# Performance work log

Hardware: AMD Instinct MI355X
Metric: run time of the kernel (lower is better)

Reference implementation:

```python
import jax, jax.numpy as jnp
import numpy as np


def setup_inputs() -> dict:
    key = jax.random.key(0)
    ks = jax.random.split(key, 7)
    B, T, IN_F = 16384, 64, 48
    F = 32          # feature_size = len(INTERACTIVE_LIST)
    H = 128         # embedding_hidden_size
    TF, TH = T * F, T * H
    scale1 = 1.0 / np.sqrt(TF)
    scale2 = 1.0 / np.sqrt(TH)
    return {
        "x": jax.random.normal(ks[0], (B, T, IN_F), dtype=jnp.float32),
        "W1": jax.random.normal(ks[1], (TF, TH), dtype=jnp.float32) * scale1,
        "b1": jax.random.normal(ks[2], (TH,), dtype=jnp.float32) * scale1,
        "W2": jax.random.normal(ks[3], (TH, TF), dtype=jnp.float32) * scale2,
        "b2": jax.random.normal(ks[4], (TF,), dtype=jnp.float32) * scale2,
        "weight": jax.random.normal(ks[5], (T, F), dtype=jnp.float32),
        "bias": jax.random.normal(ks[6], (F,), dtype=jnp.float32) * (1.0 / np.sqrt(T)),
        "sample_index": jnp.arange(F, dtype=jnp.int32),
    }


def reference(x, W1, b1, W2, b2, weight, bias, sample_index):
    # x: [B, T, IN_F]; gather interactive feature columns -> [B, T, F]
    B = x.shape[0]
    T, F = weight.shape
    xs = jnp.take(x, sample_index, axis=2)            # [B, T, F]
    # pass_linear=True path: MLP on flattened time*feature vector
    h = jax.nn.relu(xs.reshape(B, T * F) @ W1 + b1)   # [B, T*H]; dropout = identity (eval)
    out = (h @ W2 + b2).reshape(B, T, F)              # [B, T, F]
    # vectorized form of the per-sample loop: sum over time of elementwise mul
    emb = jnp.einsum("btf,tf->bf", out, weight) + bias  # [B, F]
    return emb
```

## Files before the change

kernel.cpp:

```cpp
#include <hip/hip_runtime.h>
#include <hip/hip_bf16.h>

#define BATCH 16384
#define TT    64
#define INF   48
#define FF    32
#define TFD   2048
#define THD   8192

typedef __attribute__((ext_vector_type(8))) short bf16x8;
typedef __attribute__((ext_vector_type(4))) short bf16x4;
typedef __attribute__((ext_vector_type(4))) short short4v;
typedef __attribute__((ext_vector_type(4))) float f32x4;

#define SCHED __builtin_amdgcn_sched_barrier(0)
#define VMW(n) asm volatile("s_waitcnt vmcnt(" #n ")" ::: "memory")
#define LGKM0  asm volatile("s_waitcnt lgkmcnt(0)" ::: "memory")

__device__ inline void gload_lds16(const void* g, void* l) {
  __builtin_amdgcn_global_load_lds((const __attribute__((address_space(1))) void*)g,
                                   (__attribute__((address_space(3))) void*)l, 16, 0, 0);
}

__device__ inline f32x4 mfma16x16x16_bf16(bf16x4 a, bf16x4 b, f32x4 c) {
#if __has_builtin(__builtin_amdgcn_mfma_f32_16x16x16bf16_1k)
  return __builtin_amdgcn_mfma_f32_16x16x16bf16_1k(a, b, c, 0, 0, 0);
#else
  asm("v_mfma_f32_16x16x16_bf16 %0, %1, %2, %0" : "+v"(c) : "v"(a), "v"(b));
  return c;
#endif
}

__device__ inline short f32_to_bf16_bits(float x) {
  __hip_bfloat16 h = __float2bfloat16(x);
  return *reinterpret_cast<short*>(&h);
}


__global__ void gather_cast_frag(const float* __restrict__ x, const int* __restrict__ sidx,
                                 __hip_bfloat16* __restrict__ xsf) {
  __shared__ int sx[FF];
  if (threadIdx.x < FF) sx[threadIdx.x] = sidx[threadIdx.x];
  __syncthreads();
  const int b64 = blockIdx.x >> 2;
  const int tq  = blockIdx.x & 3;
  for (int it = 0; it < 16; ++it) {
    const int slot = (tq * 16 + it) * 256 + threadIdx.x;
    const int t  = slot >> 8;
    const int bi = (slot >> 6) & 3;
    const int l  = slot & 63;
    const int lo = l & 15, hi = l >> 4;
    const int row = b64 * 64 + bi * 16 + lo;
    const float* rp = x + ((size_t)row * TT + t) * INF;
    bf16x8 v;
    #pragma unroll
    for (int j = 0; j < 8; ++j) v[j] = f32_to_bf16_bits(rp[sx[hi * 8 + j]]);
    *(bf16x8*)(xsf + ((size_t)b64 * 16384 + slot) * 8) = v;
  }
}

__global__ void transpose_w1(const float* __restrict__ W1, __hip_bfloat16* __restrict__ W1t) {
  __shared__ float tile[64][65];
  const int k0 = blockIdx.x * 64;
  const int n0 = blockIdx.y * 64;
  const int tx = threadIdx.x & 63, ty = threadIdx.x >> 6;
  for (int r = ty; r < 64; r += 4)
    tile[r][tx] = W1[(size_t)(k0 + r) * THD + n0 + tx];
  __syncthreads();
  const int rn = threadIdx.x >> 4;
  const int kq = (threadIdx.x & 15) * 4;
  for (int rr = rn; rr < 64; rr += 16) {
    short4v v;
    #pragma unroll
    for (int i = 0; i < 4; ++i) v[i] = f32_to_bf16_bits(tile[kq + i][rr]);
    *(short4v*)(W1t + (size_t)(n0 + rr) * TFD + k0 + kq) = v;
  }
}

__global__ void make_w2eff(const float* __restrict__ W2, const float* __restrict__ b2,
                           const float* __restrict__ weight, const float* __restrict__ bias,
                           __hip_bfloat16* __restrict__ w2t, float* __restrict__ beff) {
  const int n = blockIdx.x * 8 + (threadIdx.x >> 5);
  const int f = threadIdx.x & 31;
  const float* wr = W2 + (size_t)n * TFD;
  float s = 0.f;
  #pragma unroll 8
  for (int t = 0; t < TT; ++t) s += wr[t * FF + f] * weight[t * FF + f];
  w2t[(size_t)f * THD + n] = __float2bfloat16(s);
  if (blockIdx.x == 0 && threadIdx.x < FF) {
    float sb = bias[f];
    for (int t = 0; t < TT; ++t) sb += b2[t * FF + f] * weight[t * FF + f];
    beff[f] = sb;
  }
}


__device__ inline void stage_w(char* buf, const __hip_bfloat16* __restrict__ w1t,
                               int n0, int k0, int wid, int l) {
  const int sub = l >> 3;
  const int c   = (l & 7) ^ sub;
  const int h   = c >> 2, kc = c & 3;
  const int r0  = wid * 8 + sub;
  const __hip_bfloat16* gw0 = w1t + (size_t)(n0 + 2 * r0 + h) * TFD + k0 + kc * 8;
  const __hip_bfloat16* gw1 = w1t + (size_t)(n0 + 128 + 2 * r0 + h) * TFD + k0 + kc * 8;
  char* lx = buf + wid * 1024;
  gload_lds16(gw0, lx);
  gload_lds16(gw1, lx + 8192);
}

__device__ inline void stage_x(char* bufX, const char* __restrict__ xg, int t, int wid, int l) {
  const int g = wid >> 1, bi0 = (wid & 1) * 2;
  const char* src = xg + (size_t)g * 262144 + ((t * 4 + bi0) * 1024) + l * 16;
  char* dst = bufX + g * 4096 + bi0 * 1024;
  gload_lds16(src, dst);
  gload_lds16(src + 1024, dst + 1024);
}

__global__ __launch_bounds__(512, 2) void gemm_fused(
    const __hip_bfloat16* __restrict__ xsf,
    const __hip_bfloat16* __restrict__ w1t,
    const float* __restrict__ b1,
    const __hip_bfloat16* __restrict__ w2t,
    float* __restrict__ partial)
{
  __shared__ __align__(16) char lds[131072];
  const int tid = threadIdx.x;
  const int wid = tid >> 6, l = tid & 63;
  const int mq = wid >> 2, bq = wid & 3;
  const int lo = l & 15, hi = l >> 4;
  const int rl = lo >> 1;
  const int cofs = (((((lo & 1) << 2) | hi) ^ rl) << 4);
  const int strip = blockIdx.x & 7;
  const int bt = blockIdx.x >> 3;
  const int b0 = bt * 256;

  const int wbase = ((mq << 6) + rl) * 128 + cofs;
  const int xoff  = (bq << 12) + l * 16;
  const char* xg  = (const char*)xsf + (size_t)(bt * 4) * 262144;

  f32x4 acc2[2][4];
  #pragma unroll
  for (int fi = 0; fi < 2; ++fi)
    #pragma unroll
    for (int bi = 0; bi < 4; ++bi) { f32x4 z = {0.f,0.f,0.f,0.f}; acc2[fi][bi] = z; }

  for (int s = 0; s < 4; ++s) {
    const int n0 = strip * 1024 + s * 256;

    f32x4 acc[8][4];
    #pragma unroll
    for (int mi = 0; mi < 8; ++mi)
      #pragma unroll
      for (int bi = 0; bi < 4; ++bi) { f32x4 z = {0.f,0.f,0.f,0.f}; acc[mi][bi] = z; }

    stage_w(lds, w1t, n0, 0, wid, l);
    stage_x(lds + 16384, xg, 0, wid, l);
    SCHED;
    stage_w(lds + 32768, w1t, n0, 32, wid, l);
    stage_x(lds + 32768 + 16384, xg, 1, wid, l);
    SCHED;
    VMW(4); SCHED;
    __builtin_amdgcn_s_barrier(); SCHED;

    for (int t = 0; t < 64; ++t) {
      char* buf  = lds + (size_t)(t & 3) * 32768;
      char* nbuf = lds + (size_t)((t + 2) & 3) * 32768;

      bf16x8 wf0 = *(const bf16x8*)(buf + wbase);
      bf16x8 wf1 = *(const bf16x8*)(buf + wbase + 1024);
      bf16x8 wf2 = *(const bf16x8*)(buf + wbase + 2048);
      bf16x8 wf3 = *(const bf16x8*)(buf + wbase + 3072);
      bf16x8 xf0 = *(const bf16x8*)(buf + 16384 + xoff);
      bf16x8 xf1 = *(const bf16x8*)(buf + 16384 + xoff + 1024);
      bf16x8 xf2 = *(const bf16x8*)(buf + 16384 + xoff + 2048);
      bf16x8 xf3 = *(const bf16x8*)(buf + 16384 + xoff + 3072);
      if (t < 62) stage_w(nbuf, w1t, n0, (t + 2) * 32, wid, l);
      SCHED;
      __builtin_amdgcn_s_barrier();
      LGKM0; SCHED;
      __builtin_amdgcn_s_setprio(1);
      acc[0][0] = __builtin_amdgcn_mfma_f32_16x16x32_bf16(wf0, xf0, acc[0][0], 0, 0, 0);
      acc[0][1] = __builtin_amdgcn_mfma_f32_16x16x32_bf16(wf0, xf1, acc[0][1], 0, 0, 0);
      acc[0][2] = __builtin_amdgcn_mfma_f32_16x16x32_bf16(wf0, xf2, acc[0][2], 0, 0, 0);
      acc[0][3] = __builtin_amdgcn_mfma_f32_16x16x32_bf16(wf0, xf3, acc[0][3], 0, 0, 0);
      acc[1][0] = __builtin_amdgcn_mfma_f32_16x16x32_bf16(wf1, xf0, acc[1][0], 0, 0, 0);
      acc[1][1] = __builtin_amdgcn_mfma_f32_16x16x32_bf16(wf1, xf1, acc[1][1], 0, 0, 0);
      acc[1][2] = __builtin_amdgcn_mfma_f32_16x16x32_bf16(wf1, xf2, acc[1][2], 0, 0, 0);
      acc[1][3] = __builtin_amdgcn_mfma_f32_16x16x32_bf16(wf1, xf3, acc[1][3], 0, 0, 0);
      acc[2][0] = __builtin_amdgcn_mfma_f32_16x16x32_bf16(wf2, xf0, acc[2][0], 0, 0, 0);
      acc[2][1] = __builtin_amdgcn_mfma_f32_16x16x32_bf16(wf2, xf1, acc[2][1], 0, 0, 0);
      acc[2][2] = __builtin_amdgcn_mfma_f32_16x16x32_bf16(wf2, xf2, acc[2][2], 0, 0, 0);
      acc[2][3] = __builtin_amdgcn_mfma_f32_16x16x32_bf16(wf2, xf3, acc[2][3], 0, 0, 0);
      acc[3][0] = __builtin_amdgcn_mfma_f32_16x16x32_bf16(wf3, xf0, acc[3][0], 0, 0, 0);
      acc[3][1] = __builtin_amdgcn_mfma_f32_16x16x32_bf16(wf3, xf1, acc[3][1], 0, 0, 0);
      acc[3][2] = __builtin_amdgcn_mfma_f32_16x16x32_bf16(wf3, xf2, acc[3][2], 0, 0, 0);
      acc[3][3] = __builtin_amdgcn_mfma_f32_16x16x32_bf16(wf3, xf3, acc[3][3], 0, 0, 0);
      __builtin_amdgcn_s_setprio(0);
      SCHED;
      __builtin_amdgcn_s_barrier();

      bf16x8 wf4 = *(const bf16x8*)(buf + wbase + 4096);
      bf16x8 wf5 = *(const bf16x8*)(buf + wbase + 5120);
      bf16x8 wf6 = *(const bf16x8*)(buf + wbase + 6144);
      bf16x8 wf7 = *(const bf16x8*)(buf + wbase + 7168);
      if (t < 62) stage_x(nbuf + 16384, xg, t + 2, wid, l);
      SCHED;
      __builtin_amdgcn_s_barrier();
      LGKM0; SCHED;
      __builtin_amdgcn_s_setprio(1);
      acc[4][0] = __builtin_amdgcn_mfma_f32_16x16x32_bf16(wf4, xf0, acc[4][0], 0, 0, 0);
      acc[4][1] = __builtin_amdgcn_mfma_f32_16x16x32_bf16(wf4, xf1, acc[4][1], 0, 0, 0);
      acc[4][2] = __builtin_amdgcn_mfma_f32_16x16x32_bf16(wf4, xf2, acc[4][2], 0, 0, 0);
      acc[4][3] = __builtin_amdgcn_mfma_f32_16x16x32_bf16(wf4, xf3, acc[4][3], 0, 0, 0);
      acc[5][0] = __builtin_amdgcn_mfma_f32_16x16x32_bf16(wf5, xf0, acc[5][0], 0, 0, 0);
      acc[5][1] = __builtin_amdgcn_mfma_f32_16x16x32_bf16(wf5, xf1, acc[5][1], 0, 0, 0);
      acc[5][2] = __builtin_amdgcn_mfma_f32_16x16x32_bf16(wf5, xf2, acc[5][2], 0, 0, 0);
      acc[5][3] = __builtin_amdgcn_mfma_f32_16x16x32_bf16(wf5, xf3, acc[5][3], 0, 0, 0);
      acc[6][0] = __builtin_amdgcn_mfma_f32_16x16x32_bf16(wf6, xf0, acc[6][0], 0, 0, 0);
      acc[6][1] = __builtin_amdgcn_mfma_f32_16x16x32_bf16(wf6, xf1, acc[6][1], 0, 0, 0);
      acc[6][2] = __builtin_amdgcn_mfma_f32_16x16x32_bf16(wf6, xf2, acc[6][2], 0, 0, 0);
      acc[6][3] = __builtin_amdgcn_mfma_f32_16x16x32_bf16(wf6, xf3, acc[6][3], 0, 0, 0);
      acc[7][0] = __builtin_amdgcn_mfma_f32_16x16x32_bf16(wf7, xf0, acc[7][0], 0, 0, 0);
      acc[7][1] = __builtin_amdgcn_mfma_f32_16x16x32_bf16(wf7, xf1, acc[7][1], 0, 0, 0);
      acc[7][2] = __builtin_amdgcn_mfma_f32_16x16x32_bf16(wf7, xf2, acc[7][2], 0, 0, 0);
      acc[7][3] = __builtin_amdgcn_mfma_f32_16x16x32_bf16(wf7, xf3, acc[7][3], 0, 0, 0);
      __builtin_amdgcn_s_setprio(0);
      SCHED;
      if (t < 62)       { VMW(4); }
      else if (t == 62) { VMW(0); }
      SCHED;
      __builtin_amdgcn_s_barrier();
      SCHED;
    }

    #pragma unroll
    for (int mi = 0; mi < 8; ++mi) {
      const int nbase = n0 + (mq << 7) + (mi << 4);
      const float4 b1v = *(const float4*)(b1 + nbase + (hi << 2));
      bf16x4 p[4];
      #pragma unroll
      for (int bi = 0; bi < 4; ++bi) {
        bf16x4 pk;
        #pragma unroll
        for (int j = 0; j < 4; ++j) {
          float v = acc[mi][bi][j] + ((const float*)&b1v)[j];
          v = v > 0.f ? v : 0.f;
          pk[j] = f32_to_bf16_bits(v);
        }
        p[bi] = pk;
      }
      bf16x4 a2[2];
      #pragma unroll
      for (int fi = 0; fi < 2; ++fi)
        a2[fi] = *(const bf16x4*)(w2t + (size_t)(fi * 16 + lo) * THD + nbase + (hi << 2));
      #pragma unroll
      for (int fi = 0; fi < 2; ++fi)
        #pragma unroll
        for (int bi = 0; bi < 4; ++bi)
          acc2[fi][bi] = mfma16x16x16_bf16(a2[fi], p[bi], acc2[fi][bi]);
    }
  }

  float* sm = (float*)lds;
  if (mq == 1) {
    #pragma unroll
    for (int fi = 0; fi < 2; ++fi)
      #pragma unroll
      for (int bi = 0; bi < 4; ++bi)
        *(f32x4*)(sm + ((bq << 6) + (bi << 4) + lo) * 32 + fi * 16 + (hi << 2)) = acc2[fi][bi];
  }
  __syncthreads();
  if (mq == 0) {
    #pragma unroll
    for (int fi = 0; fi < 2; ++fi)
      #pragma unroll
      for (int bi = 0; bi < 4; ++bi) {
        f32x4 other = *(const f32x4*)(sm + ((bq << 6) + (bi << 4) + lo) * 32 + fi * 16 + (hi << 2));
        f32x4 v = acc2[fi][bi] + other;
        *(f32x4*)(partial + ((size_t)strip * BATCH + b0 + (bq << 6) + (bi << 4) + lo) * FF + fi * 16 + (hi << 2)) = v;
      }
  }
}

__global__ void reduce_partial(const float* __restrict__ partial, const float* __restrict__ beff,
                               float* __restrict__ out) {
  const int idx = blockIdx.x * 256 + threadIdx.x;
  float s = beff[idx & 31];
  #pragma unroll
  for (int c = 0; c < 8; ++c) s += partial[(size_t)c * BATCH * FF + idx];
  out[idx] = s;
}


extern "C" void kernel_launch(void* const* d_in, const int* in_sizes, int n_in,
                              void* d_out, int out_size, void* d_ws, size_t ws_size,
                              hipStream_t stream) {
  const float* x      = (const float*)d_in[0];
  const float* W1     = (const float*)d_in[1];
  const float* b1     = (const float*)d_in[2];
  const float* W2     = (const float*)d_in[3];
  const float* b2     = (const float*)d_in[4];
  const float* weight = (const float*)d_in[5];
  const float* bias   = (const float*)d_in[6];
  const int*   sidx   = (const int*)d_in[7];

  char* ws = (char*)d_ws;
  __hip_bfloat16* xsf  = (__hip_bfloat16*)ws;
  __hip_bfloat16* w1t  = (__hip_bfloat16*)(ws + 67108864);
  __hip_bfloat16* w2t  = (__hip_bfloat16*)(ws + 100663296);
  float*          beff = (float*)(ws + 101187584);
  float*          part = (float*)(ws + 101188608);

  hipLaunchKernelGGL(gather_cast_frag, dim3(1024), dim3(256), 0, stream, x, sidx, xsf);
  hipLaunchKernelGGL(transpose_w1, dim3(32, 128), dim3(256), 0, stream, W1, w1t);
  hipLaunchKernelGGL(make_w2eff,   dim3(1024),    dim3(256), 0, stream, W2, b2, weight, bias, w2t, beff);
  hipLaunchKernelGGL(gemm_fused,   dim3(512),     dim3(512), 0, stream, xsf, w1t, b1, w2t, part);
  hipLaunchKernelGGL(reduce_partial, dim3(2048),  dim3(256), 0, stream, part, beff, (float*)d_out);
}
```

Before: 621.3 us.

## Double waves per block to 16 and cut per-step barriers to one

Raises the fused GEMM block from 8 to 16 waves. Each wave now owns a 64-row by 64-batch tile with a 4x4 accumulator instead of 128 rows with 8x4. Every wave issues one W1 load and one X load per k-step, and both stage loads are issued at the top of the step, so the loop needs one barrier per iteration instead of three. The goal is more latency hiding and less synchronisation, at the cost of twice as many LDS reads of the X fragments and a four-way cross-wave reduction through LDS at the end.

Measured after the change: 661.2 us. +6.4%, slower.

```diff
diff --git a/kernel.cpp b/kernel.cpp
--- a/kernel.cpp
+++ b/kernel.cpp
@@ -15,7 +15,6 @@
 
 #define SCHED __builtin_amdgcn_sched_barrier(0)
 #define VMW(n) asm volatile("s_waitcnt vmcnt(" #n ")" ::: "memory")
-#define LGKM0  asm volatile("s_waitcnt lgkmcnt(0)" ::: "memory")
 
 __device__ inline void gload_lds16(const void* g, void* l) {
   __builtin_amdgcn_global_load_lds((const __attribute__((address_space(1))) void*)g,
@@ -95,28 +94,23 @@
 }
 
 
-__device__ inline void stage_w(char* buf, const __hip_bfloat16* __restrict__ w1t,
-                               int n0, int k0, int wid, int l) {
+__device__ inline void stage_w16(char* buf, const __hip_bfloat16* __restrict__ w1t,
+                                 int n0, int k0, int wid, int l) {
   const int sub = l >> 3;
   const int c   = (l & 7) ^ sub;
   const int h   = c >> 2, kc = c & 3;
   const int r0  = wid * 8 + sub;
-  const __hip_bfloat16* gw0 = w1t + (size_t)(n0 + 2 * r0 + h) * TFD + k0 + kc * 8;
-  const __hip_bfloat16* gw1 = w1t + (size_t)(n0 + 128 + 2 * r0 + h) * TFD + k0 + kc * 8;
-  char* lx = buf + wid * 1024;
-  gload_lds16(gw0, lx);
-  gload_lds16(gw1, lx + 8192);
-}
-
-__device__ inline void stage_x(char* bufX, const char* __restrict__ xg, int t, int wid, int l) {
-  const int g = wid >> 1, bi0 = (wid & 1) * 2;
-  const char* src = xg + (size_t)g * 262144 + ((t * 4 + bi0) * 1024) + l * 16;
-  char* dst = bufX + g * 4096 + bi0 * 1024;
-  gload_lds16(src, dst);
-  gload_lds16(src + 1024, dst + 1024);
-}
-
-__global__ __launch_bounds__(512, 2) void gemm_fused(
+  const __hip_bfloat16* gw = w1t + (size_t)(n0 + 2 * r0 + h) * TFD + k0 + kc * 8;
+  gload_lds16(gw, buf + wid * 1024);
+}
+
+__device__ inline void stage_x16(char* bufX, const char* __restrict__ xg, int t, int wid, int l) {
+  const int g = wid >> 2, bi = wid & 3;
+  const char* src = xg + (size_t)g * 262144 + ((t * 4 + bi) * 1024) + l * 16;
+  gload_lds16(src, bufX + wid * 1024);
+}
+
+__global__ __launch_bounds__(1024, 4) void gemm_fused(
     const __hip_bfloat16* __restrict__ xsf,
     const __hip_bfloat16* __restrict__ w1t,
     const float* __restrict__ b1,
@@ -126,7 +120,7 @@
   __shared__ __align__(16) char lds[131072];
   const int tid = threadIdx.x;
   const int wid = tid >> 6, l = tid & 63;
-  const int mq = wid >> 2, bq = wid & 3;
+  const int wn = wid >> 2, wb = wid & 3;
   const int lo = l & 15, hi = l >> 4;
   const int rl = lo >> 1;
   const int cofs = (((((lo & 1) << 2) | hi) ^ rl) << 4);
@@ -134,8 +128,8 @@
   const int bt = blockIdx.x >> 3;
   const int b0 = bt * 256;
 
-  const int wbase = ((mq << 6) + rl) * 128 + cofs;
-  const int xoff  = (bq << 12) + l * 16;
+  const int wbase = ((wn << 5) + rl) * 128 + cofs;
+  const int xoffr = 16384 + (wb << 12) + l * 16;
   const char* xg  = (const char*)xsf + (size_t)(bt * 4) * 262144;
 
   f32x4 acc2[2][4];
@@ -147,37 +141,37 @@
   for (int s = 0; s < 4; ++s) {
     const int n0 = strip * 1024 + s * 256;
 
-    f32x4 acc[8][4];
-    #pragma unroll
-    for (int mi = 0; mi < 8; ++mi)
+    f32x4 acc[4][4];
+    #pragma unroll
+    for (int mi = 0; mi < 4; ++mi)
       #pragma unroll
       for (int bi = 0; bi < 4; ++bi) { f32x4 z = {0.f,0.f,0.f,0.f}; acc[mi][bi] = z; }
 
-    stage_w(lds, w1t, n0, 0, wid, l);
-    stage_x(lds + 16384, xg, 0, wid, l);
+    stage_w16(lds, w1t, n0, 0, wid, l);
+    stage_x16(lds + 16384, xg, 0, wid, l);
     SCHED;
-    stage_w(lds + 32768, w1t, n0, 32, wid, l);
-    stage_x(lds + 32768 + 16384, xg, 1, wid, l);
+    stage_w16(lds + 32768, w1t, n0, 32, wid, l);
+    stage_x16(lds + 32768 + 16384, xg, 1, wid, l);
     SCHED;
-    VMW(4); SCHED;
+    VMW(2); SCHED;
     __builtin_amdgcn_s_barrier(); SCHED;
 
     for (int t = 0; t < 64; ++t) {
-      char* buf  = lds + (size_t)(t & 3) * 32768;
-      char* nbuf = lds + (size_t)((t + 2) & 3) * 32768;
-
+      char* buf = lds + (size_t)(t & 3) * 32768;
+      if (t <= 61) {
+        char* nbuf = lds + (size_t)((t + 2) & 3) * 32768;
+        stage_w16(nbuf, w1t, n0, (t + 2) * 32, wid, l);
+        stage_x16(nbuf + 16384, xg, t + 2, wid, l);
+      }
+      SCHED;
       bf16x8 wf0 = *(const bf16x8*)(buf + wbase);
       bf16x8 wf1 = *(const bf16x8*)(buf + wbase + 1024);
       bf16x8 wf2 = *(const bf16x8*)(buf + wbase + 2048);
       bf16x8 wf3 = *(const bf16x8*)(buf + wbase + 3072);
-      bf16x8 xf0 = *(const bf16x8*)(buf + 16384 + xoff);
-      bf16x8 xf1 = *(const bf16x8*)(buf + 16384 + xoff + 1024);
-      bf16x8 xf2 = *(const bf16x8*)(buf + 16384 + xoff + 2048);
-      bf16x8 xf3 = *(const bf16x8*)(buf + 16384 + xoff + 3072);
-      if (t < 62) stage_w(nbuf, w1t, n0, (t + 2) * 32, wid, l);
-      SCHED;
-      __builtin_amdgcn_s_barrier();
-      LGKM0; SCHED;
+      bf16x8 xf0 = *(const bf16x8*)(buf + xoffr);
+      bf16x8 xf1 = *(const bf16x8*)(buf + xoffr + 1024);
+      bf16x8 xf2 = *(const bf16x8*)(buf + xoffr + 2048);
+      bf16x8 xf3 = *(const bf16x8*)(buf + xoffr + 3072);
       __builtin_amdgcn_s_setprio(1);
       acc[0][0] = __builtin_amdgcn_mfma_f32_16x16x32_bf16(wf0, xf0, acc[0][0], 0, 0, 0);
       acc[0][1] = __builtin_amdgcn_mfma_f32_16x16x32_bf16(wf0, xf1, acc[0][1], 0, 0, 0);
@@ -197,45 +191,15 @@
       acc[3][3] = __builtin_amdgcn_mfma_f32_16x16x32_bf16(wf3, xf3, acc[3][3], 0, 0, 0);
       __builtin_amdgcn_s_setprio(0);
       SCHED;
-      __builtin_amdgcn_s_barrier();
-
-      bf16x8 wf4 = *(const bf16x8*)(buf + wbase + 4096);
-      bf16x8 wf5 = *(const bf16x8*)(buf + wbase + 5120);
-      bf16x8 wf6 = *(const bf16x8*)(buf + wbase + 6144);
-      bf16x8 wf7 = *(const bf16x8*)(buf + wbase + 7168);
-      if (t < 62) stage_x(nbuf + 16384, xg, t + 2, wid, l);
-      SCHED;
-      __builtin_amdgcn_s_barrier();
-      LGKM0; SCHED;
-      __builtin_amdgcn_s_setprio(1);
-      acc[4][0] = __builtin_amdgcn_mfma_f32_16x16x32_bf16(wf4, xf0, acc[4][0], 0, 0, 0);
-      acc[4][1] = __builtin_amdgcn_mfma_f32_16x16x32_bf16(wf4, xf1, acc[4][1], 0, 0, 0);
-      acc[4][2] = __builtin_amdgcn_mfma_f32_16x16x32_bf16(wf4, xf2, acc[4][2], 0, 0, 0);
-      acc[4][3] = __builtin_amdgcn_mfma_f32_16x16x32_bf16(wf4, xf3, acc[4][3], 0, 0, 0);
-      acc[5][0] = __builtin_amdgcn_mfma_f32_16x16x32_bf16(wf5, xf0, acc[5][0], 0, 0, 0);
-      acc[5][1] = __builtin_amdgcn_mfma_f32_16x16x32_bf16(wf5, xf1, acc[5][1], 0, 0, 0);
-      acc[5][2] = __builtin_amdgcn_mfma_f32_16x16x32_bf16(wf5, xf2, acc[5][2], 0, 0, 0);
-      acc[5][3] = __builtin_amdgcn_mfma_f32_16x16x32_bf16(wf5, xf3, acc[5][3], 0, 0, 0);
-      acc[6][0] = __builtin_amdgcn_mfma_f32_16x16x32_bf16(wf6, xf0, acc[6][0], 0, 0, 0);
-      acc[6][1] = __builtin_amdgcn_mfma_f32_16x16x32_bf16(wf6, xf1, acc[6][1], 0, 0, 0);
-      acc[6][2] = __builtin_amdgcn_mfma_f32_16x16x32_bf16(wf6, xf2, acc[6][2], 0, 0, 0);
-      acc[6][3] = __builtin_amdgcn_mfma_f32_16x16x32_bf16(wf6, xf3, acc[6][3], 0, 0, 0);
-      acc[7][0] = __builtin_amdgcn_mfma_f32_16x16x32_bf16(wf7, xf0, acc[7][0], 0, 0, 0);
-      acc[7][1] = __builtin_amdgcn_mfma_f32_16x16x32_bf16(wf7, xf1, acc[7][1], 0, 0, 0);
-      acc[7][2] = __builtin_amdgcn_mfma_f32_16x16x32_bf16(wf7, xf2, acc[7][2], 0, 0, 0);
-      acc[7][3] = __builtin_amdgcn_mfma_f32_16x16x32_bf16(wf7, xf3, acc[7][3], 0, 0, 0);
-      __builtin_amdgcn_s_setprio(0);
-      SCHED;
-      if (t < 62)       { VMW(4); }
+      if (t <= 61)      { VMW(2); }
       else if (t == 62) { VMW(0); }
       SCHED;
-      __builtin_amdgcn_s_barrier();
-      SCHED;
+      __builtin_amdgcn_s_barrier(); SCHED;
     }
 
     #pragma unroll
-    for (int mi = 0; mi < 8; ++mi) {
-      const int nbase = n0 + (mq << 7) + (mi << 4);
+    for (int mi = 0; mi < 4; ++mi) {
+      const int nbase = n0 + (wn << 6) + (mi << 4);
       const float4 b1v = *(const float4*)(b1 + nbase + (hi << 2));
       bf16x4 p[4];
       #pragma unroll
@@ -262,22 +226,27 @@
   }
 
   float* sm = (float*)lds;
-  if (mq == 1) {
+  __syncthreads();
+  if (wn != 0) {
+    float* slab = sm + (size_t)(wn - 1) * 8192;
     #pragma unroll
     for (int fi = 0; fi < 2; ++fi)
       #pragma unroll
       for (int bi = 0; bi < 4; ++bi)
-        *(f32x4*)(sm + ((bq << 6) + (bi << 4) + lo) * 32 + fi * 16 + (hi << 2)) = acc2[fi][bi];
-  }
-  __syncthreads();
-  if (mq == 0) {
+        *(f32x4*)(slab + ((wb << 6) + (bi << 4) + lo) * 32 + fi * 16 + (hi << 2)) = acc2[fi][bi];
+  }
+  __syncthreads();
+  if (wn == 0) {
     #pragma unroll
     for (int fi = 0; fi < 2; ++fi)
       #pragma unroll
       for (int bi = 0; bi < 4; ++bi) {
-        f32x4 other = *(const f32x4*)(sm + ((bq << 6) + (bi << 4) + lo) * 32 + fi * 16 + (hi << 2));
-        f32x4 v = acc2[fi][bi] + other;
-        *(f32x4*)(partial + ((size_t)strip * BATCH + b0 + (bq << 6) + (bi << 4) + lo) * FF + fi * 16 + (hi << 2)) = v;
+        const int off = ((wb << 6) + (bi << 4) + lo) * 32 + fi * 16 + (hi << 2);
+        f32x4 v = acc2[fi][bi];
+        v = v + *(const f32x4*)(sm + off);
+        v = v + *(const f32x4*)(sm + 8192 + off);
+        v = v + *(const f32x4*)(sm + 16384 + off);
+        *(f32x4*)(partial + ((size_t)strip * BATCH + b0 + (wb << 6) + (bi << 4) + lo) * FF + fi * 16 + (hi << 2)) = v;
       }
   }
 }
@@ -314,6 +283,6 @@
   hipLaunchKernelGGL(gather_cast_frag, dim3(1024), dim3(256), 0, stream, x, sidx, xsf);
   hipLaunchKernelGGL(transpose_w1, dim3(32, 128), dim3(256), 0, stream, W1, w1t);
   hipLaunchKernelGGL(make_w2eff,   dim3(1024),    dim3(256), 0, stream, W2, b2, weight, bias, w2t, beff);
-  hipLaunchKernelGGL(gemm_fused,   dim3(512),     dim3(512), 0, stream, xsf, w1t, b1, w2t, part);
+  hipLaunchKernelGGL(gemm_fused,   dim3(512),     dim3(1024), 0, stream, xsf, w1t, b1, w2t, part);
   hipLaunchKernelGGL(reduce_partial, dim3(2048),  dim3(256), 0, stream, part, beff, (float*)d_out);
 }
```
